# Kernel tuning notes

Hardware: AMD Instinct MI355X
Metric: run time of the kernel (lower is better)

## Reference

```python
import jax, jax.numpy as jnp
import numpy as np

B, N, D, H = 8, 1024, 512, 8
DH = D // H


def setup_inputs() -> dict:
    key = jax.random.key(0)
    ks = jax.random.split(key, 7)
    s = 1.0 / np.sqrt(D)
    return {
        "x": jax.random.normal(ks[0], (B, N, D), dtype=jnp.float32),
        "Wq": jax.random.normal(ks[1], (D, D), dtype=jnp.float32) * s,
        "bq": jax.random.normal(ks[2], (D,), dtype=jnp.float32) * 0.01,
        "Wk": jax.random.normal(ks[3], (D, D), dtype=jnp.float32) * s,
        "bk": jax.random.normal(ks[4], (D,), dtype=jnp.float32) * 0.01,
        "Wv": jax.random.normal(ks[5], (D, D), dtype=jnp.float32) * s,
        "bv": jax.random.normal(ks[6], (D,), dtype=jnp.float32) * 0.01,
    }


def reference(x, Wq, bq, Wk, bk, Wv, bv):
    # Q/K/V projections (nn.Linear: x @ W^T + b; here W stored as [in, out])
    q = x @ Wq + bq  # [B, N, D]
    k = x @ Wk + bk
    v = x @ Wv + bv
    # chunk(dim=2)+cat(dim=0) == split channels into H head groups
    q = q.reshape(B, N, H, DH)
    k = k.reshape(B, N, H, DH)
    v = v.reshape(B, N, H, DH)
    # NOTE: original applies NO 1/sqrt(head_dim) scaling
    scores = jnp.einsum("bqhd,bkhd->bhqk", q, k)  # [B, H, N, N]
    weights = jax.nn.softmax(scores, axis=-1)
    y = jnp.einsum("bhqk,bkhd->bqhd", weights, v)  # [B, N, H, DH]
    return y.reshape(B, N, D)
```

## Files before the change

kernel.cpp:

```cpp
#include <hip/hip_runtime.h>
#include <hip/hip_bf16.h>

typedef _Float16 half8 __attribute__((ext_vector_type(8)));
typedef _Float16 half4v __attribute__((ext_vector_type(4)));
typedef float floatx4 __attribute__((ext_vector_type(4)));

#define BB 8
#define NN 1024
#define DD 512
#define HH 8
#define DHH 64

__device__ __forceinline__ void gload_lds16(const _Float16* g, _Float16* l) {
    __builtin_amdgcn_global_load_lds(
        (const __attribute__((address_space(1))) void*)g,
        (__attribute__((address_space(3))) void*)l, 16, 0, 0);
}

__global__ __launch_bounds__(256) void cvt_kernel(const float* __restrict__ x,
                                                  const float* __restrict__ Wq,
                                                  const float* __restrict__ Wk,
                                                  const float* __restrict__ Wv,
                                                  _Float16* __restrict__ xh,
                                                  _Float16* __restrict__ Wt) {
    __shared__ __align__(16) _Float16 tb[64][72];
    int bx = blockIdx.x;
    int tid = threadIdx.x;
    if (bx < 4096) {
        int i = bx * 256 + tid;
        float4 v = ((const float4*)x)[i];
        half4v o;
        o[0] = (_Float16)v.x; o[1] = (_Float16)v.y;
        o[2] = (_Float16)v.z; o[3] = (_Float16)v.w;
        ((half4v*)xh)[i] = o;
        return;
    }
    int t = bx - 4096;
    int which = t >> 6;
    int rem = t & 63;
    int kt = (rem >> 3) * 64, nt = (rem & 7) * 64;
    const float* W = (which == 0) ? Wq : (which == 1) ? Wk : Wv;
    _Float16* Wto = Wt + (size_t)which * DD * DD;
    for (int i = 0; i < 16; i++) {
        int idx = tid + i * 256;
        int r = idx >> 6, c = idx & 63;
        tb[c][r] = (_Float16)W[(size_t)(kt + r) * DD + nt + c];
    }
    __syncthreads();
    for (int i = 0; i < 16; i++) {
        int idx = tid + i * 256;
        int r = idx >> 6, c = idx & 63;
        Wto[(size_t)(nt + r) * DD + kt + c] = tb[r][c];
    }
}

__global__ __launch_bounds__(256) void qkv_gemm_kernel(const _Float16* __restrict__ xh,
                                                       const _Float16* __restrict__ Wt,
                                                       const float* __restrict__ bq,
                                                       const float* __restrict__ bk,
                                                       const float* __restrict__ bv,
                                                       _Float16* __restrict__ QKV) {
    __shared__ __align__(16) _Float16 As[128 * 32];
    __shared__ __align__(16) _Float16 Bs[128 * 32];

    int which = blockIdx.z;
    const _Float16* Wtw = Wt + (size_t)which * DD * DD;
    const float* bias = (which == 0) ? bq : (which == 1) ? bk : bv;

    int tid = threadIdx.x;
    int wave = tid >> 6, lane = tid & 63;
    int quad = lane >> 4, l16 = lane & 15;
    int wm = wave >> 1, wn = wave & 1;
    int mBase = blockIdx.y * 128;
    int nBase = blockIdx.x * 128;

    int srow = wave * 32 + (lane >> 2);
    int scol = (lane & 3) * 8;
    const _Float16* ag = (which < 2)
        ? Wtw + (size_t)(nBase + srow) * DD + scol
        : xh  + (size_t)(mBase + srow) * DD + scol;
    const _Float16* bg = (which < 2)
        ? xh  + (size_t)(mBase + srow) * DD + scol
        : Wtw + (size_t)(nBase + srow) * DD + scol;
    _Float16* al = As + (wave * 32) * 32;
    _Float16* bl = Bs + (wave * 32) * 32;

    floatx4 acc[4][4];
    for (int i = 0; i < 4; i++)
        for (int j = 0; j < 4; j++) acc[i][j] = (floatx4){0.f, 0.f, 0.f, 0.f};

    for (int kk = 0; kk < DD; kk += 32) {
        __syncthreads();
        gload_lds16(ag + kk,            al);
        gload_lds16(ag + 16 * DD + kk,  al + 16 * 32);
        gload_lds16(bg + kk,            bl);
        gload_lds16(bg + 16 * DD + kk,  bl + 16 * 32);
        __syncthreads();

        half8 af[4], bf[4];
        for (int i = 0; i < 4; i++)
            af[i] = *(const half8*)&As[(wm * 64 + i * 16 + l16) * 32 + quad * 8];
        for (int j = 0; j < 4; j++)
            bf[j] = *(const half8*)&Bs[(wn * 64 + j * 16 + l16) * 32 + quad * 8];
        for (int i = 0; i < 4; i++)
            for (int j = 0; j < 4; j++)
                acc[i][j] = __builtin_amdgcn_mfma_f32_16x16x32_f16(af[i], bf[j], acc[i][j], 0, 0, 0);
    }

    if (which < 2) {
        _Float16* out = QKV + (size_t)which * (BB * NN) * DD;
        for (int i = 0; i < 4; i++) {
            int feat0 = nBase + wm * 64 + i * 16 + quad * 4;
            float4 b4 = *(const float4*)&bias[feat0];
            for (int j = 0; j < 4; j++) {
                int token = mBase + wn * 64 + j * 16 + l16;
                half4v pack;
                pack[0] = (_Float16)(acc[i][j][0] + b4.x);
                pack[1] = (_Float16)(acc[i][j][1] + b4.y);
                pack[2] = (_Float16)(acc[i][j][2] + b4.z);
                pack[3] = (_Float16)(acc[i][j][3] + b4.w);
                *(half4v*)&out[(size_t)token * DD + feat0] = pack;
            }
        }
    } else {
        _Float16* VT = QKV + (size_t)2 * (BB * NN) * DD;
        for (int j = 0; j < 4; j++) {
            int col = nBase + wn * 64 + j * 16 + l16;
            float bval = bias[col];
            for (int i = 0; i < 4; i++) {
                int row0 = mBase + wm * 64 + i * 16 + quad * 4;
                int b = row0 >> 10;
                int n = row0 & 1023;
                half4v pack;
                for (int reg = 0; reg < 4; reg++) pack[reg] = (_Float16)(acc[i][j][reg] + bval);
                *(half4v*)&VT[((size_t)b * 512 + col) * 1024 + n] = pack;
            }
        }
    }
}

__global__ __launch_bounds__(256) void attn_kernel(const _Float16* __restrict__ QKV,
                                                   float* __restrict__ out) {
    const _Float16* Q  = QKV;
    const _Float16* K  = QKV + (size_t)(BB * NN) * DD;
    const _Float16* VT = QKV + (size_t)2 * (BB * NN) * DD;

    __shared__ __align__(16) _Float16 Kt[128 * 64];
    __shared__ __align__(16) _Float16 Vt[64 * 128];
    __shared__ __align__(16) _Float16 PT[4][16 * 64];

    int tid = threadIdx.x;
    int wave = tid >> 6, lane = tid & 63;
    int quad = lane >> 4, l16 = lane & 15;
    int qt = blockIdx.x, h = blockIdx.y, b = blockIdx.z;

    const _Float16* Qb  = Q + ((size_t)b * NN) * DD + h * DHH;
    const _Float16* Kb  = K + ((size_t)b * NN) * DD + h * DHH;
    const _Float16* VTb = VT + ((size_t)b * 512 + h * 64) * 1024;

    int qrow = qt * 64 + wave * 16 + l16;
    half8 qf0 = *(const half8*)(Qb + (size_t)qrow * DD + 0 * 32 + quad * 8);
    half8 qf1 = *(const half8*)(Qb + (size_t)qrow * DD + 1 * 32 + quad * 8);

    floatx4 o[4];
    for (int nt = 0; nt < 4; nt++) o[nt] = (floatx4){0.f, 0.f, 0.f, 0.f};
    float m_i = -1e30f, l_i = 0.f;

    const _Float16* kg = Kb + (size_t)(wave * 32 + (lane >> 3)) * DD
                            + ((lane & 7) ^ (lane >> 3)) * 8;
    _Float16* kl = Kt + (wave * 32) * 64;
    _Float16* vl = Vt + (wave * 16) * 128;
    int l16sw = l16 & 7;

    for (int kt = 0; kt < 8; kt++) {
        __syncthreads();
        for (int i = 0; i < 4; i++)
            gload_lds16(kg + (size_t)(kt * 128 + i * 8) * DD, kl + (i * 8) * 64);
        for (int i = 0; i < 4; i++) {
            int vrow = wave * 16 + i * 4 + (lane >> 4);
            int vc = (lane & 15) ^ (i * 4 + (lane >> 4));
            gload_lds16(VTb + (size_t)vrow * 1024 + kt * 128 + vc * 8, vl + (i * 4) * 128);
        }
        __syncthreads();

        floatx4 s[8];
        for (int nt = 0; nt < 8; nt++) s[nt] = (floatx4){0.f, 0.f, 0.f, 0.f};
        for (int ks = 0; ks < 2; ks++) {
            half8 qf = ks ? qf1 : qf0;
            for (int nt = 0; nt < 8; nt++) {
                half8 kf = *(const half8*)&Kt[(nt * 16 + l16) * 64
                                              + (((ks * 4 + quad) ^ l16sw) * 8)];
                s[nt] = __builtin_amdgcn_mfma_f32_16x16x32_f16(kf, qf, s[nt], 0, 0, 0);
            }
        }

        float mx = -1e30f;
        for (int nt = 0; nt < 8; nt++)
            for (int r = 0; r < 4; r++) mx = fmaxf(mx, s[nt][r]);
        mx = fmaxf(mx, __shfl_xor(mx, 16, 64));
        mx = fmaxf(mx, __shfl_xor(mx, 32, 64));
        float mnew = fmaxf(m_i, mx);
        float alpha = __expf(m_i - mnew);
        m_i = mnew;
        float rs = 0.f;
        for (int nt = 0; nt < 8; nt++)
            for (int r = 0; r < 4; r++) {
                float p = __expf(s[nt][r] - mnew);
                s[nt][r] = p;
                rs += p;
            }
        rs += __shfl_xor(rs, 16, 64);
        rs += __shfl_xor(rs, 32, 64);
        l_i = l_i * alpha + rs;

        for (int nt = 0; nt < 4; nt++)
            for (int r = 0; r < 4; r++) o[nt][r] *= alpha;

        for (int hh = 0; hh < 2; hh++) {
            for (int ntl = 0; ntl < 4; ntl++) {
                floatx4 sv = s[hh * 4 + ntl];
                half4v p4;
                for (int r = 0; r < 4; r++) p4[r] = (_Float16)sv[r];
                *(half4v*)&PT[wave][l16 * 64 + (((2 * ntl + (quad >> 1)) ^ l16sw) * 8)
                               + (quad & 1) * 4] = p4;
            }
            for (int ks2h = 0; ks2h < 2; ks2h++) {
                half8 pf = *(const half8*)&PT[wave][l16 * 64
                                                   + (((ks2h * 4 + quad) ^ l16sw) * 8)];
                int ks2 = hh * 2 + ks2h;
                for (int nt = 0; nt < 4; nt++) {
                    half8 vf = *(const half8*)&Vt[(nt * 16 + l16) * 128
                                                  + (((ks2 * 4 + quad) ^ l16) * 8)];
                    o[nt] = __builtin_amdgcn_mfma_f32_16x16x32_f16(vf, pf, o[nt], 0, 0, 0);
                }
            }
        }
    }

    float inv = 1.0f / l_i;
    float* outb = out + ((size_t)b * NN) * DD + h * DHH;
    int row = qt * 64 + wave * 16 + l16;
    for (int nt = 0; nt < 4; nt++) {
        float4 st;
        st.x = o[nt][0] * inv; st.y = o[nt][1] * inv;
        st.z = o[nt][2] * inv; st.w = o[nt][3] * inv;
        *(float4*)&outb[(size_t)row * DD + nt * 16 + quad * 4] = st;
    }
}

extern "C" void kernel_launch(void* const* d_in, const int* in_sizes, int n_in,
                              void* d_out, int out_size, void* d_ws, size_t ws_size,
                              hipStream_t stream) {
    const float* x  = (const float*)d_in[0];
    const float* Wq = (const float*)d_in[1];
    const float* bq = (const float*)d_in[2];
    const float* Wk = (const float*)d_in[3];
    const float* bk = (const float*)d_in[4];
    const float* Wv = (const float*)d_in[5];
    const float* bv = (const float*)d_in[6];
    float* out = (float*)d_out;

    _Float16* xh  = (_Float16*)d_ws;
    _Float16* Wt  = xh + (size_t)(BB * NN) * DD;
    _Float16* QKV = Wt + (size_t)3 * DD * DD;

    hipLaunchKernelGGL(cvt_kernel, dim3(4096 + 192), dim3(256), 0, stream,
                       x, Wq, Wk, Wv, xh, Wt);
    hipLaunchKernelGGL(qkv_gemm_kernel, dim3(4, 64, 3), dim3(256), 0, stream,
                       xh, Wt, bq, bk, bv, QKV);
    hipLaunchKernelGGL(attn_kernel, dim3(16, 8, 8), dim3(256), 0, stream, QKV, out);
}
```

Before: 142.0 us.

## Double-buffer K/V LDS tiles with async prefetch in attention loop

The attention kernel now keeps two LDS buffers each for the K and V tiles. It issues the global-to-LDS loads for tile kt+1 before computing on tile kt, replacing the two barriers per iteration with one barrier at the end. The aim is to hide global-load latency behind the QK and PV MFMA work. The P fp32-to-fp16 packing also switches to the cvt_pkrtz intrinsic, which rounds toward zero instead of to nearest. The cost is doubled K/V LDS, which may lower the number of resident blocks per CU.

Result: slower. 145.5 us (+2.4%).

```diff
diff --git a/kernel.cpp b/kernel.cpp
--- a/kernel.cpp
+++ b/kernel.cpp
@@ -145,8 +145,8 @@
     const _Float16* K  = QKV + (size_t)(BB * NN) * DD;
     const _Float16* VT = QKV + (size_t)2 * (BB * NN) * DD;
 
-    __shared__ __align__(16) _Float16 Kt[128 * 64];
-    __shared__ __align__(16) _Float16 Vt[64 * 128];
+    __shared__ __align__(16) _Float16 Kt[2][128 * 64];
+    __shared__ __align__(16) _Float16 Vt[2][64 * 128];
     __shared__ __align__(16) _Float16 PT[4][16 * 64];
 
     int tid = threadIdx.x;
@@ -168,28 +168,46 @@
 
     const _Float16* kg = Kb + (size_t)(wave * 32 + (lane >> 3)) * DD
                             + ((lane & 7) ^ (lane >> 3)) * 8;
-    _Float16* kl = Kt + (wave * 32) * 64;
-    _Float16* vl = Vt + (wave * 16) * 128;
     int l16sw = l16 & 7;
 
-    for (int kt = 0; kt < 8; kt++) {
-        __syncthreads();
+    {
+        _Float16* kl = Kt[0] + (wave * 32) * 64;
+        _Float16* vl = Vt[0] + (wave * 16) * 128;
         for (int i = 0; i < 4; i++)
-            gload_lds16(kg + (size_t)(kt * 128 + i * 8) * DD, kl + (i * 8) * 64);
+            gload_lds16(kg + (size_t)(i * 8) * DD, kl + (i * 8) * 64);
         for (int i = 0; i < 4; i++) {
             int vrow = wave * 16 + i * 4 + (lane >> 4);
             int vc = (lane & 15) ^ (i * 4 + (lane >> 4));
-            gload_lds16(VTb + (size_t)vrow * 1024 + kt * 128 + vc * 8, vl + (i * 4) * 128);
-        }
-        __syncthreads();
+            gload_lds16(VTb + (size_t)vrow * 1024 + vc * 8, vl + (i * 4) * 128);
+        }
+    }
+    __syncthreads();
+
+    for (int kt = 0; kt < 8; kt++) {
+        int cur = kt & 1, nxt = cur ^ 1;
+        if (kt < 7) {
+            _Float16* kl = Kt[nxt] + (wave * 32) * 64;
+            _Float16* vl = Vt[nxt] + (wave * 16) * 128;
+            for (int i = 0; i < 4; i++)
+                gload_lds16(kg + (size_t)((kt + 1) * 128 + i * 8) * DD, kl + (i * 8) * 64);
+            for (int i = 0; i < 4; i++) {
+                int vrow = wave * 16 + i * 4 + (lane >> 4);
+                int vc = (lane & 15) ^ (i * 4 + (lane >> 4));
+                gload_lds16(VTb + (size_t)vrow * 1024 + (kt + 1) * 128 + vc * 8,
+                            vl + (i * 4) * 128);
+            }
+        }
+
+        const _Float16* Ktc = Kt[cur];
+        const _Float16* Vtc = Vt[cur];
 
         floatx4 s[8];
         for (int nt = 0; nt < 8; nt++) s[nt] = (floatx4){0.f, 0.f, 0.f, 0.f};
         for (int ks = 0; ks < 2; ks++) {
             half8 qf = ks ? qf1 : qf0;
             for (int nt = 0; nt < 8; nt++) {
-                half8 kf = *(const half8*)&Kt[(nt * 16 + l16) * 64
-                                              + (((ks * 4 + quad) ^ l16sw) * 8)];
+                half8 kf = *(const half8*)&Ktc[(nt * 16 + l16) * 64
+                                               + (((ks * 4 + quad) ^ l16sw) * 8)];
                 s[nt] = __builtin_amdgcn_mfma_f32_16x16x32_f16(kf, qf, s[nt], 0, 0, 0);
             }
         }
@@ -219,22 +237,24 @@
         for (int hh = 0; hh < 2; hh++) {
             for (int ntl = 0; ntl < 4; ntl++) {
                 floatx4 sv = s[hh * 4 + ntl];
-                half4v p4;
-                for (int r = 0; r < 4; r++) p4[r] = (_Float16)sv[r];
-                *(half4v*)&PT[wave][l16 * 64 + (((2 * ntl + (quad >> 1)) ^ l16sw) * 8)
-                               + (quad & 1) * 4] = p4;
+                int d0 = __builtin_bit_cast(int, __builtin_amdgcn_cvt_pkrtz(sv[0], sv[1]));
+                int d1 = __builtin_bit_cast(int, __builtin_amdgcn_cvt_pkrtz(sv[2], sv[3]));
+                int2 wv = make_int2(d0, d1);
+                *(int2*)&PT[wave][l16 * 64 + (((2 * ntl + (quad >> 1)) ^ l16sw) * 8)
+                               + (quad & 1) * 4] = wv;
             }
             for (int ks2h = 0; ks2h < 2; ks2h++) {
                 half8 pf = *(const half8*)&PT[wave][l16 * 64
                                                    + (((ks2h * 4 + quad) ^ l16sw) * 8)];
                 int ks2 = hh * 2 + ks2h;
                 for (int nt = 0; nt < 4; nt++) {
-                    half8 vf = *(const half8*)&Vt[(nt * 16 + l16) * 128
-                                                  + (((ks2 * 4 + quad) ^ l16) * 8)];
+                    half8 vf = *(const half8*)&Vtc[(nt * 16 + l16) * 128
+                                                   + (((ks2 * 4 + quad) ^ l16) * 8)];
                     o[nt] = __builtin_amdgcn_mfma_f32_16x16x32_f16(vf, pf, o[nt], 0, 0, 0);
                 }
             }
         }
+        __syncthreads();
     }
 
     float inv = 1.0f / l_i;
```

## Double-buffer QKV GEMM with swizzled 64-wide K tiles and packed P conversion

Applied to the files above, without the earlier changes.

The QKV projection GEMM now uses a 64-wide K tile with two LDS buffers. The next tile's global-to-LDS load is issued before computing on the current one, and there is one barrier per iteration instead of two. The LDS layout uses an XOR swizzle on 16-byte chunks to avoid bank conflicts on the MFMA fragment reads. Separately, the attention P-matrix fp16 conversion uses packed round-toward-zero conversion instructions. Together these double LDS usage per block, which may reduce occupancy, and round-toward-zero slightly changes numerics.

Result: slower. 147.4 us (+3.8%).

```diff
diff --git a/kernel.cpp b/kernel.cpp
--- a/kernel.cpp
+++ b/kernel.cpp
@@ -60,8 +60,8 @@
                                                        const float* __restrict__ bk,
                                                        const float* __restrict__ bv,
                                                        _Float16* __restrict__ QKV) {
-    __shared__ __align__(16) _Float16 As[128 * 32];
-    __shared__ __align__(16) _Float16 Bs[128 * 32];
+    __shared__ __align__(16) _Float16 As[2][128 * 64];
+    __shared__ __align__(16) _Float16 Bs[2][128 * 64];
 
     int which = blockIdx.z;
     const _Float16* Wtw = Wt + (size_t)which * DD * DD;
@@ -74,37 +74,59 @@
     int mBase = blockIdx.y * 128;
     int nBase = blockIdx.x * 128;
 
-    int srow = wave * 32 + (lane >> 2);
-    int scol = (lane & 3) * 8;
+    int srow = wave * 32 + (lane >> 3);
+    int scol = ((lane & 7) ^ (lane >> 3)) * 8;
     const _Float16* ag = (which < 2)
         ? Wtw + (size_t)(nBase + srow) * DD + scol
         : xh  + (size_t)(mBase + srow) * DD + scol;
     const _Float16* bg = (which < 2)
         ? xh  + (size_t)(mBase + srow) * DD + scol
         : Wtw + (size_t)(nBase + srow) * DD + scol;
-    _Float16* al = As + (wave * 32) * 32;
-    _Float16* bl = Bs + (wave * 32) * 32;
 
     floatx4 acc[4][4];
     for (int i = 0; i < 4; i++)
         for (int j = 0; j < 4; j++) acc[i][j] = (floatx4){0.f, 0.f, 0.f, 0.f};
 
-    for (int kk = 0; kk < DD; kk += 32) {
+    int l16sw = l16 & 7;
+
+    {
+        _Float16* al = As[0] + (wave * 32) * 64;
+        _Float16* bl = Bs[0] + (wave * 32) * 64;
+        for (int i = 0; i < 4; i++) {
+            gload_lds16(ag + (size_t)(i * 8) * DD, al + (i * 8) * 64);
+            gload_lds16(bg + (size_t)(i * 8) * DD, bl + (i * 8) * 64);
+        }
+    }
+    __syncthreads();
+
+    for (int kt = 0; kt < 8; kt++) {
+        int cur = kt & 1, nxt = cur ^ 1;
+        if (kt < 7) {
+            int kk = (kt + 1) * 64;
+            _Float16* al = As[nxt] + (wave * 32) * 64;
+            _Float16* bl = Bs[nxt] + (wave * 32) * 64;
+            for (int i = 0; i < 4; i++) {
+                gload_lds16(ag + (size_t)(i * 8) * DD + kk, al + (i * 8) * 64);
+                gload_lds16(bg + (size_t)(i * 8) * DD + kk, bl + (i * 8) * 64);
+            }
+        }
+        const _Float16* Ac = As[cur];
+        const _Float16* Bc = Bs[cur];
+
+        for (int ks = 0; ks < 2; ks++) {
+            half8 af[4], bf[4];
+            for (int i = 0; i < 4; i++)
+                af[i] = *(const half8*)&Ac[(wm * 64 + i * 16 + l16) * 64
+                                           + (((ks * 4 + quad) ^ l16sw) * 8)];
+            for (int j = 0; j < 4; j++)
+                bf[j] = *(const half8*)&Bc[(wn * 64 + j * 16 + l16) * 64
+                                           + (((ks * 4 + quad) ^ l16sw) * 8)];
+            for (int i = 0; i < 4; i++)
+                for (int j = 0; j < 4; j++)
+                    acc[i][j] = __builtin_amdgcn_mfma_f32_16x16x32_f16(af[i], bf[j],
+                                                                       acc[i][j], 0, 0, 0);
+        }
         __syncthreads();
-        gload_lds16(ag + kk,            al);
-        gload_lds16(ag + 16 * DD + kk,  al + 16 * 32);
-        gload_lds16(bg + kk,            bl);
-        gload_lds16(bg + 16 * DD + kk,  bl + 16 * 32);
-        __syncthreads();
-
-        half8 af[4], bf[4];
-        for (int i = 0; i < 4; i++)
-            af[i] = *(const half8*)&As[(wm * 64 + i * 16 + l16) * 32 + quad * 8];
-        for (int j = 0; j < 4; j++)
-            bf[j] = *(const half8*)&Bs[(wn * 64 + j * 16 + l16) * 32 + quad * 8];
-        for (int i = 0; i < 4; i++)
-            for (int j = 0; j < 4; j++)
-                acc[i][j] = __builtin_amdgcn_mfma_f32_16x16x32_f16(af[i], bf[j], acc[i][j], 0, 0, 0);
     }
 
     if (which < 2) {
@@ -219,10 +241,11 @@
         for (int hh = 0; hh < 2; hh++) {
             for (int ntl = 0; ntl < 4; ntl++) {
                 floatx4 sv = s[hh * 4 + ntl];
-                half4v p4;
-                for (int r = 0; r < 4; r++) p4[r] = (_Float16)sv[r];
-                *(half4v*)&PT[wave][l16 * 64 + (((2 * ntl + (quad >> 1)) ^ l16sw) * 8)
-                               + (quad & 1) * 4] = p4;
+                int d0 = __builtin_bit_cast(int, __builtin_amdgcn_cvt_pkrtz(sv[0], sv[1]));
+                int d1 = __builtin_bit_cast(int, __builtin_amdgcn_cvt_pkrtz(sv[2], sv[3]));
+                int2 wv = make_int2(d0, d1);
+                *(int2*)&PT[wave][l16 * 64 + (((2 * ntl + (quad >> 1)) ^ l16sw) * 8)
+                               + (quad & 1) * 4] = wv;
             }
             for (int ks2h = 0; ks2h < 2; ks2h++) {
                 half8 pf = *(const half8*)&PT[wave][l16 * 64
```

## Process two query tiles per wave in attention to reuse K/V loads

Applied to the files above, without the earlier changes.

Each wave now handles 32 query rows (two 16-row MFMA tiles), so a block covers 128 queries and the grid halves. Each K/V tile loaded into LDS and each fragment read from it now feed two MFMAs, halving global K/V traffic and LDS reads per query. The grid order is swapped so the head index varies fastest, and the P conversion to fp16 uses packed cvt_pkrtz instructions. The cost is higher register pressure, more LDS for P, and fewer blocks (512), which may lower occupancy.

New measurement: 151.1 us. 6.4% more time.

```diff
diff --git a/kernel.cpp b/kernel.cpp
--- a/kernel.cpp
+++ b/kernel.cpp
@@ -147,24 +147,31 @@
 
     __shared__ __align__(16) _Float16 Kt[128 * 64];
     __shared__ __align__(16) _Float16 Vt[64 * 128];
-    __shared__ __align__(16) _Float16 PT[4][16 * 64];
+    __shared__ __align__(16) _Float16 PT[4][32 * 64];
 
     int tid = threadIdx.x;
     int wave = tid >> 6, lane = tid & 63;
     int quad = lane >> 4, l16 = lane & 15;
-    int qt = blockIdx.x, h = blockIdx.y, b = blockIdx.z;
+    int h = blockIdx.x, qt = blockIdx.y, b = blockIdx.z;
 
     const _Float16* Qb  = Q + ((size_t)b * NN) * DD + h * DHH;
     const _Float16* Kb  = K + ((size_t)b * NN) * DD + h * DHH;
     const _Float16* VTb = VT + ((size_t)b * 512 + h * 64) * 1024;
 
-    int qrow = qt * 64 + wave * 16 + l16;
-    half8 qf0 = *(const half8*)(Qb + (size_t)qrow * DD + 0 * 32 + quad * 8);
-    half8 qf1 = *(const half8*)(Qb + (size_t)qrow * DD + 1 * 32 + quad * 8);
-
-    floatx4 o[4];
-    for (int nt = 0; nt < 4; nt++) o[nt] = (floatx4){0.f, 0.f, 0.f, 0.f};
-    float m_i = -1e30f, l_i = 0.f;
+    int qrow0 = qt * 128 + wave * 32 + l16;
+    int qrow1 = qrow0 + 16;
+    half8 qf[2][2];
+    qf[0][0] = *(const half8*)(Qb + (size_t)qrow0 * DD + 0 * 32 + quad * 8);
+    qf[0][1] = *(const half8*)(Qb + (size_t)qrow0 * DD + 1 * 32 + quad * 8);
+    qf[1][0] = *(const half8*)(Qb + (size_t)qrow1 * DD + 0 * 32 + quad * 8);
+    qf[1][1] = *(const half8*)(Qb + (size_t)qrow1 * DD + 1 * 32 + quad * 8);
+
+    floatx4 o0[4], o1[4];
+    for (int nt = 0; nt < 4; nt++) {
+        o0[nt] = (floatx4){0.f, 0.f, 0.f, 0.f};
+        o1[nt] = (floatx4){0.f, 0.f, 0.f, 0.f};
+    }
+    float m0 = -1e30f, l0 = 0.f, m1 = -1e30f, l1 = 0.f;
 
     const _Float16* kg = Kb + (size_t)(wave * 32 + (lane >> 3)) * DD
                             + ((lane & 7) ^ (lane >> 3)) * 8;
@@ -183,68 +190,108 @@
         }
         __syncthreads();
 
-        floatx4 s[8];
-        for (int nt = 0; nt < 8; nt++) s[nt] = (floatx4){0.f, 0.f, 0.f, 0.f};
+        floatx4 s0[8], s1[8];
+        for (int nt = 0; nt < 8; nt++) {
+            s0[nt] = (floatx4){0.f, 0.f, 0.f, 0.f};
+            s1[nt] = (floatx4){0.f, 0.f, 0.f, 0.f};
+        }
         for (int ks = 0; ks < 2; ks++) {
-            half8 qf = ks ? qf1 : qf0;
             for (int nt = 0; nt < 8; nt++) {
                 half8 kf = *(const half8*)&Kt[(nt * 16 + l16) * 64
                                               + (((ks * 4 + quad) ^ l16sw) * 8)];
-                s[nt] = __builtin_amdgcn_mfma_f32_16x16x32_f16(kf, qf, s[nt], 0, 0, 0);
-            }
-        }
-
-        float mx = -1e30f;
-        for (int nt = 0; nt < 8; nt++)
-            for (int r = 0; r < 4; r++) mx = fmaxf(mx, s[nt][r]);
-        mx = fmaxf(mx, __shfl_xor(mx, 16, 64));
-        mx = fmaxf(mx, __shfl_xor(mx, 32, 64));
-        float mnew = fmaxf(m_i, mx);
-        float alpha = __expf(m_i - mnew);
-        m_i = mnew;
-        float rs = 0.f;
-        for (int nt = 0; nt < 8; nt++)
-            for (int r = 0; r < 4; r++) {
-                float p = __expf(s[nt][r] - mnew);
-                s[nt][r] = p;
-                rs += p;
-            }
-        rs += __shfl_xor(rs, 16, 64);
-        rs += __shfl_xor(rs, 32, 64);
-        l_i = l_i * alpha + rs;
-
-        for (int nt = 0; nt < 4; nt++)
-            for (int r = 0; r < 4; r++) o[nt][r] *= alpha;
+                s0[nt] = __builtin_amdgcn_mfma_f32_16x16x32_f16(kf, qf[0][ks], s0[nt], 0, 0, 0);
+                s1[nt] = __builtin_amdgcn_mfma_f32_16x16x32_f16(kf, qf[1][ks], s1[nt], 0, 0, 0);
+            }
+        }
+
+        {
+            float mx = -1e30f;
+            for (int nt = 0; nt < 8; nt++)
+                for (int r = 0; r < 4; r++) mx = fmaxf(mx, s0[nt][r]);
+            mx = fmaxf(mx, __shfl_xor(mx, 16, 64));
+            mx = fmaxf(mx, __shfl_xor(mx, 32, 64));
+            float mnew = fmaxf(m0, mx);
+            float alpha = __expf(m0 - mnew);
+            m0 = mnew;
+            float rs = 0.f;
+            for (int nt = 0; nt < 8; nt++)
+                for (int r = 0; r < 4; r++) {
+                    float p = __expf(s0[nt][r] - mnew);
+                    s0[nt][r] = p;
+                    rs += p;
+                }
+            rs += __shfl_xor(rs, 16, 64);
+            rs += __shfl_xor(rs, 32, 64);
+            l0 = l0 * alpha + rs;
+            for (int nt = 0; nt < 4; nt++)
+                for (int r = 0; r < 4; r++) o0[nt][r] *= alpha;
+        }
+        {
+            float mx = -1e30f;
+            for (int nt = 0; nt < 8; nt++)
+                for (int r = 0; r < 4; r++) mx = fmaxf(mx, s1[nt][r]);
+            mx = fmaxf(mx, __shfl_xor(mx, 16, 64));
+            mx = fmaxf(mx, __shfl_xor(mx, 32, 64));
+            float mnew = fmaxf(m1, mx);
+            float alpha = __expf(m1 - mnew);
+            m1 = mnew;
+            float rs = 0.f;
+            for (int nt = 0; nt < 8; nt++)
+                for (int r = 0; r < 4; r++) {
+                    float p = __expf(s1[nt][r] - mnew);
+                    s1[nt][r] = p;
+                    rs += p;
+                }
+            rs += __shfl_xor(rs, 16, 64);
+            rs += __shfl_xor(rs, 32, 64);
+            l1 = l1 * alpha + rs;
+            for (int nt = 0; nt < 4; nt++)
+                for (int r = 0; r < 4; r++) o1[nt][r] *= alpha;
+        }
 
         for (int hh = 0; hh < 2; hh++) {
             for (int ntl = 0; ntl < 4; ntl++) {
-                floatx4 sv = s[hh * 4 + ntl];
-                half4v p4;
-                for (int r = 0; r < 4; r++) p4[r] = (_Float16)sv[r];
-                *(half4v*)&PT[wave][l16 * 64 + (((2 * ntl + (quad >> 1)) ^ l16sw) * 8)
-                               + (quad & 1) * 4] = p4;
+                floatx4 sv = s0[hh * 4 + ntl];
+                int d0 = __builtin_bit_cast(int, __builtin_amdgcn_cvt_pkrtz(sv[0], sv[1]));
+                int d1 = __builtin_bit_cast(int, __builtin_amdgcn_cvt_pkrtz(sv[2], sv[3]));
+                *(int2*)&PT[wave][l16 * 64 + (((2 * ntl + (quad >> 1)) ^ l16sw) * 8)
+                               + (quad & 1) * 4] = make_int2(d0, d1);
+                sv = s1[hh * 4 + ntl];
+                d0 = __builtin_bit_cast(int, __builtin_amdgcn_cvt_pkrtz(sv[0], sv[1]));
+                d1 = __builtin_bit_cast(int, __builtin_amdgcn_cvt_pkrtz(sv[2], sv[3]));
+                *(int2*)&PT[wave][(16 + l16) * 64 + (((2 * ntl + (quad >> 1)) ^ l16sw) * 8)
+                               + (quad & 1) * 4] = make_int2(d0, d1);
             }
             for (int ks2h = 0; ks2h < 2; ks2h++) {
-                half8 pf = *(const half8*)&PT[wave][l16 * 64
-                                                   + (((ks2h * 4 + quad) ^ l16sw) * 8)];
+                half8 pf0 = *(const half8*)&PT[wave][l16 * 64
+                                                    + (((ks2h * 4 + quad) ^ l16sw) * 8)];
+                half8 pf1 = *(const half8*)&PT[wave][(16 + l16) * 64
+                                                    + (((ks2h * 4 + quad) ^ l16sw) * 8)];
                 int ks2 = hh * 2 + ks2h;
                 for (int nt = 0; nt < 4; nt++) {
                     half8 vf = *(const half8*)&Vt[(nt * 16 + l16) * 128
                                                   + (((ks2 * 4 + quad) ^ l16) * 8)];
-                    o[nt] = __builtin_amdgcn_mfma_f32_16x16x32_f16(vf, pf, o[nt], 0, 0, 0);
+                    o0[nt] = __builtin_amdgcn_mfma_f32_16x16x32_f16(vf, pf0, o0[nt], 0, 0, 0);
+                    o1[nt] = __builtin_amdgcn_mfma_f32_16x16x32_f16(vf, pf1, o1[nt], 0, 0, 0);
                 }
             }
         }
     }
 
-    float inv = 1.0f / l_i;
     float* outb = out + ((size_t)b * NN) * DD + h * DHH;
-    int row = qt * 64 + wave * 16 + l16;
+    float inv0 = 1.0f / l0;
     for (int nt = 0; nt < 4; nt++) {
         float4 st;
-        st.x = o[nt][0] * inv; st.y = o[nt][1] * inv;
-        st.z = o[nt][2] * inv; st.w = o[nt][3] * inv;
-        *(float4*)&outb[(size_t)row * DD + nt * 16 + quad * 4] = st;
+        st.x = o0[nt][0] * inv0; st.y = o0[nt][1] * inv0;
+        st.z = o0[nt][2] * inv0; st.w = o0[nt][3] * inv0;
+        *(float4*)&outb[(size_t)qrow0 * DD + nt * 16 + quad * 4] = st;
+    }
+    float inv1 = 1.0f / l1;
+    for (int nt = 0; nt < 4; nt++) {
+        float4 st;
+        st.x = o1[nt][0] * inv1; st.y = o1[nt][1] * inv1;
+        st.z = o1[nt][2] * inv1; st.w = o1[nt][3] * inv1;
+        *(float4*)&outb[(size_t)qrow1 * DD + nt * 16 + quad * 4] = st;
     }
 }
 
@@ -268,5 +315,5 @@
                        x, Wq, Wk, Wv, xh, Wt);
     hipLaunchKernelGGL(qkv_gemm_kernel, dim3(4, 64, 3), dim3(256), 0, stream,
                        xh, Wt, bq, bk, bv, QKV);
-    hipLaunchKernelGGL(attn_kernel, dim3(16, 8, 8), dim3(256), 0, stream, QKV, out);
-}
+    hipLaunchKernelGGL(attn_kernel, dim3(8, 8, 8), dim3(256), 0, stream, QKV, out);
+}
```
